# Performance work log

Hardware: AMD Instinct MI355X
Metric: run time of the kernel (lower is better)

Reference implementation:

```python
import jax, jax.numpy as jnp
import numpy as np

N = 50000      # num nodes
E = 40000      # num edges (multiple of BATCH)
BATCH = 200    # hardcoded edge batch size in source
ND, ED, TD, MD, D = 256, 128, 128, 256, 256
P = 4096       # num post nodes
EPS = 1e-16


def setup_inputs() -> dict:
    key = jax.random.key(0)
    ks = jax.random.split(key, 24)
    s = 0.02
    inp = {}
    inp["node_features"] = jax.random.normal(ks[0], (N, ND), jnp.float32)
    inp["edge_index"] = jax.random.randint(ks[1], (2, E), 0, N, jnp.int32)
    inp["edge_attr"] = jax.random.normal(ks[2], (E, ED), jnp.float32)
    inp["edge_times"] = jax.random.uniform(ks[3], (E,), jnp.float32)
    inp["post_mask"] = jax.random.randint(ks[4], (P,), 0, N, jnp.int32)
    # TimeEncoder('sin') params
    inp["w_time"] = jnp.ones((TD,), jnp.float32)
    inp["b_time"] = jnp.zeros((TD,), jnp.float32)
    # message_fn: Linear(ND+MD+ED+TD -> D), ReLU, Linear(D -> MD), ReLU
    min_dim = ND + MD + ED + TD
    inp["Wm1"] = s * jax.random.normal(ks[5], (min_dim, D), jnp.float32)
    inp["bm1"] = jnp.zeros((D,), jnp.float32)
    inp["Wm2"] = s * jax.random.normal(ks[6], (D, MD), jnp.float32)
    inp["bm2"] = jnp.zeros((MD,), jnp.float32)
    # GRUCell(MD, MD)
    inp["Wi"] = s * jax.random.normal(ks[7], (MD, 3 * MD), jnp.float32)
    inp["Wh"] = s * jax.random.normal(ks[8], (MD, 3 * MD), jnp.float32)
    inp["bi"] = jnp.zeros((3 * MD,), jnp.float32)
    inp["bh"] = jnp.zeros((3 * MD,), jnp.float32)
    # graph attention embedding: in = ND+MD+TD (augmented), edge feat = ED+TD
    inp["Wg"] = s * jax.random.normal(ks[9], (ND + MD + TD, D), jnp.float32)
    inp["We"] = s * jax.random.normal(ks[10], (ED + TD, D), jnp.float32)
    inp["a_src"] = s * jax.random.normal(ks[11], (D,), jnp.float32)
    inp["a_dst"] = s * jax.random.normal(ks[12], (D,), jnp.float32)
    inp["a_e"] = s * jax.random.normal(ks[13], (D,), jnp.float32)
    # classifier MLP: Linear(D -> D//2), ReLU, Linear(D//2 -> 1)
    inp["Wc1"] = s * jax.random.normal(ks[14], (D, D // 2), jnp.float32)
    inp["bc1"] = jnp.zeros((D // 2,), jnp.float32)
    inp["Wc2"] = s * jax.random.normal(ks[15], (D // 2, 1), jnp.float32)
    inp["bc2"] = jnp.zeros((1,), jnp.float32)
    return inp


def reference(node_features, edge_index, edge_attr, edge_times, post_mask,
              w_time, b_time, Wm1, bm1, Wm2, bm2, Wi, Wh, bi, bh,
              Wg, We, a_src, a_dst, a_e, Wc1, bc1, Wc2, bc2):
    def time_enc(t):  # TimeEncoder 'sin': sin(w * t + b)
        return jnp.sin(t[..., None] * w_time + b_time)

    # ---- time-sorted edge stream, batched in chunks of BATCH ----
    order = jnp.argsort(edge_times)
    nb = E // BATCH
    src_s = edge_index[0, order].reshape(nb, BATCH)
    ea_s = edge_attr[order].reshape(nb, BATCH, ED)
    t_s = edge_times[order].reshape(nb, BATCH)

    def step(mem, batch):
        src, ea, t = batch
        te = time_enc(t)                                   # [B, TD]
        h_prev = mem[src]                                  # [B, MD]
        x = jnp.concatenate([node_features[src], h_prev, ea, te], axis=-1)
        msg = jax.nn.relu(jax.nn.relu(x @ Wm1 + bm1) @ Wm2 + bm2)  # [B, MD]
        gi = msg @ Wi + bi
        gh = h_prev @ Wh + bh
        ir, iz, inn = jnp.split(gi, 3, axis=-1)
        hr, hz, hn = jnp.split(gh, 3, axis=-1)
        r = jax.nn.sigmoid(ir + hr)
        z = jax.nn.sigmoid(iz + hz)
        n = jnp.tanh(inn + r * hn)
        h_new = (1.0 - z) * n + z * h_prev
        mem = mem.at[src].set(h_new)
        return mem, None

    mem0 = jnp.zeros((N, MD), jnp.float32)
    mem, _ = jax.lax.scan(step, mem0, (src_s, ea_s, t_s))

    # ---- augmented node features with global time encoding ----
    gte = time_enc(jnp.max(edge_times))                    # [TD]
    gte = jnp.broadcast_to(gte, (N, TD))
    aug = jnp.concatenate([node_features, mem, gte], axis=1)  # [N, ND+MD+TD]

    # ---- graph attention embedding (single layer) ----
    h = aug @ Wg                                           # [N, D]
    ef = jnp.concatenate([edge_attr, time_enc(edge_times)], axis=1) @ We  # [E, D]
    s_idx, d_idx = edge_index[0], edge_index[1]
    logit = jax.nn.leaky_relu(
        (h @ a_src)[s_idx] + (h @ a_dst)[d_idx] + ef @ a_e, 0.2)  # [E]
    mx = jax.ops.segment_max(logit, d_idx, num_segments=N)
    mx = jnp.where(jnp.isfinite(mx), mx, 0.0)
    alpha = jnp.exp(logit - mx[d_idx])
    denom = jax.ops.segment_sum(alpha, d_idx, num_segments=N)     # [N]
    msg = alpha[:, None] * (h[s_idx] + ef)                        # [E, D]
    out = jax.ops.segment_sum(msg, d_idx, num_segments=N) / (denom[:, None] + EPS)

    # ---- classifier head on post nodes ----
    pe = out[post_mask]                                    # [P, D]
    logits = (jax.nn.relu(pe @ Wc1 + bc1) @ Wc2 + bc2)[:, 0]
    return jax.nn.sigmoid(logits)
```

## Files before the change

kernel.cpp:

```cpp
#include <hip/hip_runtime.h>

#define NN 50000
#define EE 40000
#define PP 4096
#define MAXR 12
#define SCAP 16
#define NB 65536
#define TANCH 2
#define TSTEPS 10
#define TGRID 512

typedef unsigned short us;
typedef __attribute__((ext_vector_type(8))) short bf8v;
typedef __attribute__((ext_vector_type(4))) float f4v;

__device__ __forceinline__ us f2b(float x) {
    unsigned u = __float_as_uint(x);
    u = (u + 0x7fffu + ((u >> 16) & 1u)) >> 16;
    return (us)u;
}
__device__ __forceinline__ float b2f(us h) {
    return __uint_as_float(((unsigned)h) << 16);
}
__device__ __forceinline__ unsigned fkey(float f) {
    unsigned u = __float_as_uint(f);
    return (u & 0x80000000u) ? ~u : (u | 0x80000000u);
}
__device__ __forceinline__ float funkey(unsigned k) {
    unsigned u = (k & 0x80000000u) ? (k & 0x7fffffffu) : ~k;
    return __uint_as_float(u);
}
__device__ __forceinline__ int bucket_of(float tv) {
    int b = (int)(tv * 65536.0f);
    if (b < 0) b = 0;
    if (b > 65535) b = 65535;
    return b;
}
__device__ __forceinline__ unsigned relu2bf(unsigned u) {
    unsigned lo = (u & 0x8000u) ? 0u : (u & 0xFFFFu);
    unsigned hi = (u & 0x80000000u) ? 0u : (u & 0xFFFF0000u);
    return lo | hi;
}


__global__ void k_need(const int* __restrict__ pm, int* __restrict__ needed)
{
    int i = blockIdx.x * 256 + threadIdx.x;
    if (i < PP) needed[pm[i]] = 1;
}

__global__ void k_elist(const int* __restrict__ src, const int* __restrict__ dst,
                        const int* __restrict__ needed, int* __restrict__ necnt,
                        int* __restrict__ eidx, int* __restrict__ uneed)
{
    __shared__ int lc, lb;
    if (threadIdx.x == 0) lc = 0;
    __syncthreads();
    int e = blockIdx.x * 256 + threadIdx.x;
    int slot = -1;
    if (e < EE && needed[dst[e]]) {
        slot = atomicAdd(&lc, 1);
        uneed[dst[e]] = 1;
        uneed[src[e]] = 1;
    }
    __syncthreads();
    if (threadIdx.x == 0 && lc) lb = atomicAdd(necnt, lc);
    __syncthreads();
    if (slot >= 0) eidx[lb + slot] = e;
}

__global__ void k_ulist(const int* __restrict__ uneed, int* __restrict__ ucnt,
                        int* __restrict__ ulist, int* __restrict__ nidx)
{
    __shared__ int lc, lb;
    if (threadIdx.x == 0) lc = 0;
    __syncthreads();
    int n = blockIdx.x * 256 + threadIdx.x;
    int slot = -1;
    if (n < NN && uneed[n]) slot = atomicAdd(&lc, 1);
    __syncthreads();
    if (threadIdx.x == 0 && lc) lb = atomicAdd(ucnt, lc);
    __syncthreads();
    if (slot >= 0) { ulist[lb + slot] = n; nidx[n] = lb + slot; }
}


__global__ __launch_bounds__(256) void k_prep(const float* __restrict__ t, const int* __restrict__ src,
                                              int* __restrict__ hist, int* __restrict__ scnt,
                                              int* __restrict__ slist, unsigned* __restrict__ tm)
{
    int e = blockIdx.x * 256 + threadIdx.x;
    float v = 0.f;
    if (e < EE) {
        float tv = t[e];
        v = tv;
        atomicAdd(&hist[bucket_of(tv)], 1);
        int s = src[e];
        int slot = atomicAdd(&scnt[s], 1);
        if (slot < SCAP) slist[s * SCAP + slot] = e;
    }
#pragma unroll
    for (int o = 32; o > 0; o >>= 1) v = fmaxf(v, __shfl_xor(v, o));
    if ((threadIdx.x & 63) == 0) atomicMax(tm, fkey(v));
}

__global__ void k_scan1(const int* __restrict__ hist, int* __restrict__ hbase, int* __restrict__ bsum)
{
    __shared__ int s[256];
    int i = blockIdx.x * 256 + threadIdx.x;
    int v = hist[i];
    s[threadIdx.x] = v;
    __syncthreads();
    for (int o = 1; o < 256; o <<= 1) {
        int x = (threadIdx.x >= o) ? s[threadIdx.x - o] : 0;
        __syncthreads();
        s[threadIdx.x] += x;
        __syncthreads();
    }
    hbase[i] = s[threadIdx.x] - v;
    if (threadIdx.x == 255) bsum[blockIdx.x] = s[255];
}

__global__ void k_scan2(int* __restrict__ bsum)
{
    __shared__ int s[256];
    int v = bsum[threadIdx.x];
    s[threadIdx.x] = v;
    __syncthreads();
    for (int o = 1; o < 256; o <<= 1) {
        int x = (threadIdx.x >= o) ? s[threadIdx.x - o] : 0;
        __syncthreads();
        s[threadIdx.x] += x;
        __syncthreads();
    }
    bsum[threadIdx.x] = s[threadIdx.x] - v;
}

__global__ void k_scan3(int* __restrict__ hbase, const int* __restrict__ bsum)
{
    int i = blockIdx.x * 256 + threadIdx.x;
    hbase[i] += bsum[blockIdx.x];
}

__global__ void k_bscatter(const float* __restrict__ t, const int* __restrict__ hbase,
                           int* __restrict__ hcur, int* __restrict__ blist)
{
    int e = blockIdx.x * 256 + threadIdx.x;
    if (e >= EE) return;
    int b = bucket_of(t[e]);
    int p = hbase[b] + atomicAdd(&hcur[b], 1);
    blist[p] = e;
}

__global__ void k_rank2(const float* __restrict__ t, const int* __restrict__ hbase,
                        const int* __restrict__ hist, const int* __restrict__ blist,
                        int* __restrict__ rank)
{
    int e = blockIdx.x * 256 + threadIdx.x;
    if (e >= EE) return;
    float te_ = t[e];
    int b = bucket_of(te_);
    int base = hbase[b], cnt = hist[b];
    int r = base;
    for (int i = 0; i < cnt; ++i) {
        int j = blist[base + i];
        float tj = t[j];
        r += (tj < te_ || (tj == te_ && j < e)) ? 1 : 0;
    }
    rank[e] = r;
}

__global__ void k_chain(const int* __restrict__ src, const int* __restrict__ rank,
                        const int* __restrict__ scnt, const int* __restrict__ slist,
                        const int* __restrict__ uneed,
                        int* __restrict__ roundcnt, int* __restrict__ roundx, int* __restrict__ roundsrc,
                        int* __restrict__ xcnt, int* __restrict__ xlist, int* __restrict__ xsrc)
{
    __shared__ int lcnt[MAXR];
    __shared__ int lbase[MAXR];
    __shared__ int xl, xb;
    int tid = threadIdx.x;
    if (tid < MAXR) lcnt[tid] = 0;
    if (tid == 0) xl = 0;
    __syncthreads();
    int e = blockIdx.x * 256 + tid;
    int pos = -1, slot = 0, xs = 0, ssave = 0;
    if (e < EE && uneed[src[e]]) {
        int s = src[e];
        int c = scnt[s]; if (c > SCAP) c = SCAP;
        int re = rank[e], be = re / 200;
        bool r_e = true;
        for (int i = 0; i < c; ++i) {
            int rj = rank[slist[s * SCAP + i]];
            if (rj / 200 == be && rj > re) { r_e = false; break; }
        }
        if (r_e) {
            int p = 0;
            for (int i = 0; i < c; ++i) {
                int rj = rank[slist[s * SCAP + i]];
                if (rj >= re) continue;
                int bj = rj / 200;
                bool r_j = true;
                for (int k2 = 0; k2 < c; ++k2) {
                    int rj2 = rank[slist[s * SCAP + k2]];
                    if (rj2 / 200 == bj && rj2 > rj) { r_j = false; break; }
                }
                p += r_j ? 1 : 0;
            }
            if (p < MAXR) { pos = p; ssave = s; slot = atomicAdd(&lcnt[p], 1); xs = atomicAdd(&xl, 1); }
        }
    }
    __syncthreads();
    if (tid < MAXR && lcnt[tid]) lbase[tid] = atomicAdd(&roundcnt[tid], lcnt[tid]);
    if (tid == 0 && xl) xb = atomicAdd(xcnt, xl);
    __syncthreads();
    if (pos >= 0) {
        int xr = xb + xs;
        xlist[xr] = e;
        xsrc[xr] = ssave;
        size_t o = (size_t)pos * EE + lbase[pos] + slot;
        roundx[o] = xr;
        roundsrc[o] = ssave;
    }
}


__global__ void k_zmem(const int* __restrict__ ucnt, const int* __restrict__ ulist,
                       float* __restrict__ memb, us* __restrict__ memb_bf)
{
    int total = *ucnt * 64;
    for (int i = blockIdx.x * 256 + threadIdx.x; i < total; i += gridDim.x * 256) {
        int n = ulist[i >> 6], q = i & 63;
        reinterpret_cast<float4*>(memb + (size_t)n * 256)[q] = make_float4(0.f, 0.f, 0.f, 0.f);
        reinterpret_cast<ushort4*>(memb_bf + (size_t)n * 256)[q] = make_ushort4(0, 0, 0, 0);
    }
}

__global__ void k_cvtg(const int* __restrict__ ucnt, const int* __restrict__ ulist,
                       const float* __restrict__ nf, us* __restrict__ nf_bf)
{
    int total = *ucnt * 64;
    for (int i = blockIdx.x * 256 + threadIdx.x; i < total; i += gridDim.x * 256) {
        int n = ulist[i >> 6], q = i & 63;
        float4 v = reinterpret_cast<const float4*>(nf + (size_t)n * 256)[q];
        ushort4 o; o.x = f2b(v.x); o.y = f2b(v.y); o.z = f2b(v.z); o.w = f2b(v.w);
        reinterpret_cast<ushort4*>(nf_bf + (size_t)n * 256)[q] = o;
    }
}

__global__ void k_convL(const int* __restrict__ cnt, const int* __restrict__ list,
                        const float* __restrict__ t, const float* __restrict__ w,
                        const float* __restrict__ b, us* __restrict__ te,
                        const float* __restrict__ ea, us* __restrict__ ea_bf)
{
    int total = *cnt * 32;
    for (int i = blockIdx.x * 256 + threadIdx.x; i < total; i += gridDim.x * 256) {
        int e = list[i >> 5], q = (i & 31) * 4;
        float tv = t[e];
        ushort4 ot;
        ot.x = f2b(sinf(tv * w[q] + b[q]));
        ot.y = f2b(sinf(tv * w[q + 1] + b[q + 1]));
        ot.z = f2b(sinf(tv * w[q + 2] + b[q + 2]));
        ot.w = f2b(sinf(tv * w[q + 3] + b[q + 3]));
        *reinterpret_cast<ushort4*>(te + (size_t)e * 128 + q) = ot;
        float4 v = *reinterpret_cast<const float4*>(ea + (size_t)e * 128 + q);
        ushort4 oa; oa.x = f2b(v.x); oa.y = f2b(v.y); oa.z = f2b(v.z); oa.w = f2b(v.w);
        *reinterpret_cast<ushort4*>(ea_bf + (size_t)e * 128 + q) = oa;
    }
}

__global__ void k_zout(const int* __restrict__ pm, float* __restrict__ outb,
                       float* __restrict__ denom, unsigned* __restrict__ mx)
{
    int i = blockIdx.x * 256 + threadIdx.x;
    int p = i >> 6, q = i & 63;
    if (p >= PP) return;
    int n = pm[p];
    reinterpret_cast<float4*>(outb + (size_t)n * 256)[q] = make_float4(0.f, 0.f, 0.f, 0.f);
    if (q == 0) { denom[n] = 0.f; mx[n] = 0u; }
}

__global__ void k_wkflat(const float* __restrict__ sa, us* __restrict__ da, int na4,
                         const float* __restrict__ sb, us* __restrict__ db, int nb4,
                         const float* __restrict__ sc, us* __restrict__ dc, int nc4,
                         const float* __restrict__ sd, us* __restrict__ dd, int nd4)
{
    int i = blockIdx.x * 256 + threadIdx.x;
    const float* sp; us* dp; int j = i;
    if (j < na4) { sp = sa; dp = da; }
    else { j -= na4; if (j < nb4) { sp = sb; dp = db; }
    else { j -= nb4; if (j < nc4) { sp = sc; dp = dc; }
    else { j -= nc4; if (j < nd4) { sp = sd; dp = dd; } else return; } } }
    float4 v = reinterpret_cast<const float4*>(sp)[j];
    ushort4 o; o.x = f2b(v.x); o.y = f2b(v.y); o.z = f2b(v.z); o.w = f2b(v.w);
    reinterpret_cast<ushort4*>(dp)[j] = o;
}


struct WtD { const float* W; us* dst; int K, N, ld, koff, Ktot, toff; };
struct WtA { WtD d[12]; int ntiles; };

__global__ __launch_bounds__(256) void k_wt2(WtA wa, const unsigned* __restrict__ tm,
                                             const float* __restrict__ wt, const float* __restrict__ bt,
                                             const float* __restrict__ Wg, float* __restrict__ gvec)
{
    if ((int)blockIdx.x == wa.ntiles) {
        __shared__ float sv[128];
        int c = threadIdx.x;
        float tmax = funkey(*tm);
        if (c < 128) sv[c] = sinf(tmax * wt[c] + bt[c]);
        __syncthreads();
        float acc = 0.f;
        for (int k = 0; k < 128; ++k) acc += sv[k] * Wg[(size_t)(512 + k) * 256 + c];
        gvec[c] = acc;
        return;
    }
    int bid = blockIdx.x;
    int di = 0;
#pragma unroll
    for (int i = 1; i < 12; ++i) if (bid >= wa.d[i].toff) di = i;
    WtD d = wa.d[di];
    int tt = bid - d.toff;
    int tn = d.N >> 5;
    int k0 = (tt / tn) << 5, n0 = (tt % tn) << 5;
    __shared__ float ld[32][33];
    int tx = threadIdx.x & 31, ty = threadIdx.x >> 5;
#pragma unroll
    for (int i = 0; i < 4; ++i)
        ld[ty + 8 * i][tx] = d.W[(size_t)(k0 + ty + 8 * i) * d.ld + n0 + tx];
    __syncthreads();
#pragma unroll
    for (int i = 0; i < 4; ++i) {
        int n = n0 + ty + 8 * i;
        d.dst[(size_t)n * d.Ktot + d.koff + k0 + tx] = f2b(ld[tx][ty + 8 * i]);
    }
}

__global__ __launch_bounds__(256) void k_mgemm(
    const us* __restrict__ A1, int K1, const int* __restrict__ idx1,
    const us* __restrict__ A2, int K2, const int* __restrict__ idx2,
    const us* __restrict__ A3, int K3, const int* __restrict__ idx3,
    const us* __restrict__ Wt, int Kloop, int ldw,
    const float* __restrict__ bias,
    const us* __restrict__ Cin, const int* __restrict__ cidx,
    float* __restrict__ outF, us* __restrict__ outB, int ldc,
    int Mhost, const int* __restrict__ mdev, int mbase, int relu, int relua)
{
    int M = Mhost;
    if (mdev) {
        int avail = *mdev - mbase;
        if (avail < 0) avail = 0;
        if (avail < M) M = avail;
    }
    const int row0 = blockIdx.x * 128;
    if (row0 >= M) return;
    const int col0 = blockIdx.y * 64;

    __shared__ us As[128 * 64];
    __shared__ us Bs[64 * 64];

    const int tid = threadIdx.x;
    const int l = tid & 63;
    const int wv = tid >> 6;

    f4v acc[2][4];
#pragma unroll
    for (int i = 0; i < 2; ++i)
#pragma unroll
        for (int j = 0; j < 4; ++j) acc[i][j] = (f4v){0.f, 0.f, 0.f, 0.f};

    for (int k0 = 0; k0 < Kloop; k0 += 64) {
#pragma unroll
        for (int it = 0; it < 4; ++it) {
            int idx = tid + it * 256;
            int r = idx >> 3, q = idx & 7;
            int gk = k0 + q * 8;
            int grow = row0 + r;
            uint4 v = make_uint4(0u, 0u, 0u, 0u);
            if (grow < M) {
                const us* sp; int st, krel, ar = grow;
                if (gk < K1) {
                    sp = A1; st = K1; krel = gk;
                    if (idx1) ar = idx1[ar];
                } else if (gk < K1 + K2) {
                    sp = A2; st = K2; krel = gk - K1;
                    if (idx2) ar = idx2[ar];
                } else {
                    sp = A3; st = K3; krel = gk - K1 - K2;
                    if (idx3) ar = idx3[ar];
                }
                v = *reinterpret_cast<const uint4*>(sp + (size_t)ar * st + krel);
                if (relua) { v.x = relu2bf(v.x); v.y = relu2bf(v.y); v.z = relu2bf(v.z); v.w = relu2bf(v.w); }
            }
            *reinterpret_cast<uint4*>(As + r * 64 + ((q ^ (r & 7)) << 3)) = v;
        }
#pragma unroll
        for (int it = 0; it < 2; ++it) {
            int idx = tid + it * 256;
            int c = idx >> 3, q = idx & 7;
            uint4 v = *reinterpret_cast<const uint4*>(Wt + (size_t)(col0 + c) * ldw + k0 + q * 8);
            *reinterpret_cast<uint4*>(Bs + c * 64 + ((q ^ (c & 7)) << 3)) = v;
        }
        __syncthreads();
#pragma unroll
        for (int ks = 0; ks < 2; ++ks) {
            bf8v af[2], bfr[4];
#pragma unroll
            for (int mf = 0; mf < 2; ++mf) {
                int r = wv * 32 + mf * 16 + (l & 15);
                int q = ks * 4 + (l >> 4);
                af[mf] = *reinterpret_cast<const bf8v*>(As + r * 64 + ((q ^ (r & 7)) << 3));
            }
#pragma unroll
            for (int nf = 0; nf < 4; ++nf) {
                int c = nf * 16 + (l & 15);
                int q = ks * 4 + (l >> 4);
                bfr[nf] = *reinterpret_cast<const bf8v*>(Bs + c * 64 + ((q ^ (c & 7)) << 3));
            }
#pragma unroll
            for (int mf = 0; mf < 2; ++mf)
#pragma unroll
                for (int nf = 0; nf < 4; ++nf)
                    acc[mf][nf] = __builtin_amdgcn_mfma_f32_16x16x32_bf16(af[mf], bfr[nf], acc[mf][nf], 0, 0, 0);
        }
        __syncthreads();
    }

#pragma unroll
    for (int mf = 0; mf < 2; ++mf) {
#pragma unroll
        for (int rr = 0; rr < 4; ++rr) {
            int row = row0 + wv * 32 + mf * 16 + ((l >> 4) * 4) + rr;
            if (row >= M) continue;
            size_t crow = 0;
            if (Cin) crow = (size_t)(cidx ? cidx[row] : row) * ldc;
#pragma unroll
            for (int nf = 0; nf < 4; ++nf) {
                int col = col0 + nf * 16 + (l & 15);
                float v = acc[mf][nf][rr];
                if (bias) v += bias[col];
                if (Cin) v += b2f(Cin[crow + col]);
                if (relu) v = fmaxf(v, 0.f);
                if (outF) outF[(size_t)row * ldc + col] = v;
                if (outB) outB[(size_t)row * ldc + col] = f2b(v);
            }
        }
    }
}


__global__ void k_hgather(const int* __restrict__ cnt, int cb, int m, const int* __restrict__ rs,
                          const us* __restrict__ mem_bf, us* __restrict__ hprev)
{
    int idx = blockIdx.x * 256 + threadIdx.x;
    int i = idx >> 6, q = idx & 63;
    int avail = *cnt - cb;
    if (avail > m) avail = m;
    if (i >= avail) return;
    int s = rs[i];
    reinterpret_cast<ushort4*>(hprev + (size_t)i * 256)[q] =
        reinterpret_cast<const ushort4*>(mem_bf + (size_t)s * 256)[q];
}

__global__ void k_gate(const int* __restrict__ cnt, int cb, int m, const int* __restrict__ rs,
                       const us* __restrict__ gates, const float* __restrict__ bi,
                       const float* __restrict__ bh,
                       float* __restrict__ mem, us* __restrict__ mem_bf)
{
    int avail = *cnt - cb;
    if (avail > m) avail = m;
    int c = threadIdx.x;
    for (int i = blockIdx.x; i < avail; i += gridDim.x) {
        int s = rs[i];
        float hp = mem[(size_t)s * 256 + c];
        const us* g = gates + (size_t)i * 1024;
        float g0 = b2f(g[c]) + bi[c] + bh[c];
        float g1 = b2f(g[256 + c]) + bi[256 + c] + bh[256 + c];
        float g2i = b2f(g[512 + c]) + bi[512 + c];
        float g2h = b2f(g[768 + c]) + bh[512 + c];
        float r = 1.f / (1.f + expf(-g0));
        float z = 1.f / (1.f + expf(-g1));
        float n = tanhf(g2i + r * g2h);
        float hnew = (1.f - z) * n + z * hp;
        mem[(size_t)s * 256 + c] = hnew;
        mem_bf[(size_t)s * 256 + c] = f2b(hnew);
    }
}

__global__ void k_tbuild(const int* __restrict__ roundcnt, const int* __restrict__ roundx,
                         const int* __restrict__ roundsrc, int* __restrict__ tx)
{
    int i = blockIdx.x * 256 + threadIdx.x;
    if (i >= roundcnt[TANCH]) return;
    int s = roundsrc[(size_t)TANCH * EE + i];
    tx[i * TSTEPS + 0] = roundx[(size_t)TANCH * EE + i];
#pragma unroll
    for (int k = 1; k < TSTEPS; ++k) tx[i * TSTEPS + k] = -1;
    for (int j = TANCH + 1; j < MAXR; ++j) {
        int cj = roundcnt[j];
        for (int m2 = 0; m2 < cj; ++m2) {
            if (roundsrc[(size_t)j * EE + m2] == s) {
                tx[i * TSTEPS + (j - TANCH)] = roundx[(size_t)j * EE + m2];
                break;
            }
        }
    }
}

__global__ __launch_bounds__(1024) void k_tailchain(
    const int* __restrict__ roundcnt, const int* __restrict__ roundsrc, const int* __restrict__ tx,
    const us* __restrict__ xpart_c, const us* __restrict__ Wk_a, const us* __restrict__ Wk_m2,
    const us* __restrict__ Wk_i, const us* __restrict__ Wk_h, const float* __restrict__ bm2,
    const float* __restrict__ bi, const float* __restrict__ bh,
    float* __restrict__ mem, us* __restrict__ mem_bf)
{
    const int cnt = roundcnt[TANCH];
    const int tid = threadIdx.x;
    const int c = tid & 255;
    const int p = tid >> 8;
    __shared__ float hb[256];
    __shared__ float xv[256];
    __shared__ float msgv[256];
    __shared__ float red[4][256];
    __shared__ float oi[768];
    __shared__ float oh[768];
    for (int i = blockIdx.x; i < cnt; i += gridDim.x) {
        int s = roundsrc[(size_t)TANCH * EE + i];
        float hp = 0.f;
        if (p == 0) { hp = mem[(size_t)s * 256 + c]; hb[c] = hp; }
        __syncthreads();
        for (int k = 0; k < TSTEPS; ++k) {
            int xr = tx[i * TSTEPS + k];
            if (xr < 0) break;
            {
                float a = 0.f;
                int k0 = p * 64;
#pragma unroll 16
                for (int kk = 0; kk < 64; ++kk) a += b2f(Wk_a[(size_t)(k0 + kk) * 256 + c]) * hb[k0 + kk];
                red[p][c] = a;
            }
            __syncthreads();
            if (p == 0)
                xv[c] = fmaxf(b2f(xpart_c[(size_t)xr * 256 + c]) + red[0][c] + red[1][c] + red[2][c] + red[3][c], 0.f);
            __syncthreads();
            {
                float a = 0.f;
                int k0 = p * 64;
#pragma unroll 16
                for (int kk = 0; kk < 64; ++kk) a += b2f(Wk_m2[(size_t)(k0 + kk) * 256 + c]) * xv[k0 + kk];
                red[p][c] = a;
            }
            __syncthreads();
            if (p == 0)
                msgv[c] = fmaxf(bm2[c] + red[0][c] + red[1][c] + red[2][c] + red[3][c], 0.f);
            __syncthreads();
            if (tid < 768) {
                float a = 0.f;
#pragma unroll 16
                for (int kk = 0; kk < 256; ++kk) a += b2f(Wk_i[(size_t)kk * 768 + tid]) * msgv[kk];
                oi[tid] = a;
            } else {
                int j = tid - 768;
                float a = 0.f;
#pragma unroll 16
                for (int kk = 0; kk < 256; ++kk) a += b2f(Wk_h[(size_t)kk * 768 + j]) * hb[kk];
                oh[j] = a;
            }
            if (tid < 512) {
                int j = 256 + tid;
                float a = 0.f;
#pragma unroll 16
                for (int kk = 0; kk < 256; ++kk) a += b2f(Wk_h[(size_t)kk * 768 + j]) * hb[kk];
                oh[j] = a;
            }
            __syncthreads();
            if (p == 0) {
                float r = 1.f / (1.f + expf(-(oi[c] + oh[c] + bi[c] + bh[c])));
                float z = 1.f / (1.f + expf(-(oi[256 + c] + oh[256 + c] + bi[256 + c] + bh[256 + c])));
                float n = tanhf((oi[512 + c] + bi[512 + c]) + r * (oh[512 + c] + bh[512 + c]));
                hp = (1.f - z) * n + z * hp;
                hb[c] = hp;
            }
            __syncthreads();
        }
        if (p == 0) {
            mem[(size_t)s * 256 + c] = hp;
            mem_bf[(size_t)s * 256 + c] = f2b(hp);
        }
        __syncthreads();
    }
}


__global__ __launch_bounds__(256) void k_dots(const us* __restrict__ hc, const us* __restrict__ efc,
                                              const int* __restrict__ ucnt, const int* __restrict__ necnt,
                                              const float* __restrict__ v_s, const float* __restrict__ v_d,
                                              const float* __restrict__ v_e,
                                              float* __restrict__ sdot, float* __restrict__ ddot,
                                              float* __restrict__ edot)
{
    int lane = threadIdx.x & 63;
    int row = blockIdx.x * 4 + (threadIdx.x >> 6);
    if (row < NN) {
        if (row >= *ucnt) return;
        ushort4 q = reinterpret_cast<const ushort4*>(hc + (size_t)row * 256)[lane];
        int c = lane * 4;
        float x0 = b2f(q.x), x1 = b2f(q.y), x2 = b2f(q.z), x3 = b2f(q.w);
        float s1 = x0 * v_s[c] + x1 * v_s[c + 1] + x2 * v_s[c + 2] + x3 * v_s[c + 3];
        float s2 = x0 * v_d[c] + x1 * v_d[c + 1] + x2 * v_d[c + 2] + x3 * v_d[c + 3];
#pragma unroll
        for (int o = 32; o > 0; o >>= 1) { s1 += __shfl_xor(s1, o); s2 += __shfl_xor(s2, o); }
        if (lane == 0) { sdot[row] = s1; ddot[row] = s2; }
    } else {
        int i = row - NN;
        if (i >= *necnt) return;
        ushort4 q = reinterpret_cast<const ushort4*>(efc + (size_t)i * 256)[lane];
        int c = lane * 4;
        float s1 = b2f(q.x) * v_e[c] + b2f(q.y) * v_e[c + 1] + b2f(q.z) * v_e[c + 2] + b2f(q.w) * v_e[c + 3];
#pragma unroll
        for (int o = 32; o > 0; o >>= 1) s1 += __shfl_xor(s1, o);
        if (lane == 0) edot[i] = s1;
    }
}

__global__ void k_logitc(const int* __restrict__ necnt, const int* __restrict__ eidx,
                         const int* __restrict__ nidx,
                         const float* __restrict__ sdot, const float* __restrict__ ddot,
                         const float* __restrict__ edot, const int* __restrict__ src,
                         const int* __restrict__ dst, float* __restrict__ logit,
                         unsigned* __restrict__ mx)
{
    int i = blockIdx.x * 256 + threadIdx.x;
    if (i >= *necnt) return;
    int e = eidx[i];
    float l = sdot[nidx[src[e]]] + ddot[nidx[dst[e]]] + edot[i];
    l = (l > 0.f) ? l : 0.2f * l;
    logit[i] = l;
    atomicMax(&mx[dst[e]], fkey(l));
}

__global__ void k_alphac(const int* __restrict__ necnt, const int* __restrict__ eidx,
                         const float* __restrict__ logit, const int* __restrict__ dst,
                         const unsigned* __restrict__ mx, float* __restrict__ alpha,
                         float* __restrict__ denom)
{
    int i = blockIdx.x * 256 + threadIdx.x;
    if (i >= *necnt) return;
    int d = dst[eidx[i]];
    float a = expf(logit[i] - funkey(mx[d]));
    alpha[i] = a;
    atomicAdd(&denom[d], a);
}

__global__ void k_scatc(const int* __restrict__ necnt, const int* __restrict__ eidx,
                        const int* __restrict__ nidx,
                        const float* __restrict__ alpha, const int* __restrict__ src,
                        const int* __restrict__ dst, const us* __restrict__ hc,
                        const us* __restrict__ efc, float* __restrict__ outb)
{
    int i = blockIdx.x * 4 + (threadIdx.x >> 6);
    if (i >= *necnt) return;
    int c4 = threadIdx.x & 63;
    int e = eidx[i];
    float a = alpha[i];
    ushort4 hv = reinterpret_cast<const ushort4*>(hc + (size_t)nidx[src[e]] * 256)[c4];
    ushort4 ev = reinterpret_cast<const ushort4*>(efc + (size_t)i * 256)[c4];
    float* op = outb + (size_t)dst[e] * 256 + c4 * 4;
    atomicAdd(op + 0, a * (b2f(hv.x) + b2f(ev.x)));
    atomicAdd(op + 1, a * (b2f(hv.y) + b2f(ev.y)));
    atomicAdd(op + 2, a * (b2f(hv.z) + b2f(ev.z)));
    atomicAdd(op + 3, a * (b2f(hv.w) + b2f(ev.w)));
}

__global__ void k_pe(const int* __restrict__ pm, const float* __restrict__ outb,
                     const float* __restrict__ denom, us* __restrict__ pe)
{
    int p = blockIdx.x, c = threadIdx.x;
    int n = pm[p];
    pe[(size_t)p * 256 + c] = f2b(outb[(size_t)n * 256 + c] / (denom[n] + 1e-16f));
}

__global__ __launch_bounds__(256) void k_final(const float* __restrict__ c1, const float* __restrict__ Wc2,
                                               const float* __restrict__ bc2, float* __restrict__ out)
{
    int lane = threadIdx.x & 63;
    int row = blockIdx.x * 4 + (threadIdx.x >> 6);
    if (row >= PP) return;
    float s = 0.f;
    for (int c = lane; c < 128; c += 64) s += c1[(size_t)row * 128 + c] * Wc2[c];
#pragma unroll
    for (int off = 32; off > 0; off >>= 1) s += __shfl_xor(s, off);
    if (lane == 0) out[row] = 1.f / (1.f + expf(-(s + bc2[0])));
}


extern "C" void kernel_launch(void* const* d_in, const int* in_sizes, int n_in,
                              void* d_out, int out_size, void* d_ws, size_t ws_size,
                              hipStream_t stream)
{
    (void)in_sizes; (void)n_in; (void)out_size;
    const float* nf    = (const float*)d_in[0];
    const int*   ei    = (const int*)  d_in[1];
    const float* ea    = (const float*)d_in[2];
    const float* t     = (const float*)d_in[3];
    const int*   pm    = (const int*)  d_in[4];
    const float* wt    = (const float*)d_in[5];
    const float* bt    = (const float*)d_in[6];
    const float* Wm1   = (const float*)d_in[7];
    const float* bm1   = (const float*)d_in[8];
    const float* Wm2   = (const float*)d_in[9];
    const float* bm2   = (const float*)d_in[10];
    const float* Wi    = (const float*)d_in[11];
    const float* Wh    = (const float*)d_in[12];
    const float* bi    = (const float*)d_in[13];
    const float* bh    = (const float*)d_in[14];
    const float* Wg    = (const float*)d_in[15];
    const float* We    = (const float*)d_in[16];
    const float* a_src = (const float*)d_in[17];
    const float* a_dst = (const float*)d_in[18];
    const float* a_e   = (const float*)d_in[19];
    const float* Wc1   = (const float*)d_in[20];
    const float* bc1   = (const float*)d_in[21];
    const float* Wc2   = (const float*)d_in[22];
    const float* bc2   = (const float*)d_in[23];
    float* outp = (float*)d_out;
    const int* src = ei;
    const int* dst = ei + EE;

    char* base = (char*)d_ws;
    size_t off = 0;
    auto alloc = [&](size_t bytes) -> void* {
        void* p = base + off;
        off = (off + bytes + 255) & ~(size_t)255;
        return p;
    };
    int* rank      = (int*)alloc((size_t)EE * 4);
    int* roundcnt  = (int*)alloc(64 * 4);
    int* roundx    = (int*)alloc((size_t)MAXR * EE * 4);
    int* roundsrc  = (int*)alloc((size_t)MAXR * EE * 4);
    int* bsum      = (int*)alloc(256 * 4);
    int* eidx      = (int*)alloc((size_t)EE * 4);
    int* xlist     = (int*)alloc((size_t)EE * 4);
    int* xsrc      = (int*)alloc((size_t)EE * 4);
    int* tx        = (int*)alloc((size_t)TSTEPS * (EE / 3 + 256) * 4);
    int* ulist     = (int*)alloc((size_t)NN * 4);
    int* nidx      = (int*)alloc((size_t)NN * 4);
    us* te_bf    = (us*)alloc((size_t)EE * 128 * 2);
    us* nf_bf    = (us*)alloc((size_t)NN * 256 * 2);
    us* ea_bf    = (us*)alloc((size_t)EE * 128 * 2);
    us* xh       = (us*)alloc((size_t)NN * 256 * 2);
    float* memb  = (float*)alloc((size_t)NN * 256 * 4);
    us* memb_bf  = (us*)alloc((size_t)NN * 256 * 2);
    us* Wt_x    = (us*)alloc((size_t)256 * 512 * 2);
    us* Wt_a    = (us*)alloc((size_t)256 * 256 * 2);
    us* Wt_m2   = (us*)alloc((size_t)256 * 256 * 2);
    us* Wt_gate = (us*)alloc((size_t)1024 * 512 * 2);
    us* Wt_g    = (us*)alloc((size_t)256 * 512 * 2);
    us* Wt_e    = (us*)alloc((size_t)256 * 256 * 2);
    us* Wt_c    = (us*)alloc((size_t)128 * 256 * 2);
    us* Wk_a    = (us*)alloc((size_t)256 * 256 * 2);
    us* Wk_m2   = (us*)alloc((size_t)256 * 256 * 2);
    us* Wk_i    = (us*)alloc((size_t)256 * 768 * 2);
    us* Wk_h    = (us*)alloc((size_t)256 * 768 * 2);
    float* gvec  = (float*)alloc(256 * 4);
    float* sdot  = (float*)alloc((size_t)NN * 4);
    float* ddot  = (float*)alloc((size_t)NN * 4);
    float* edot  = (float*)alloc((size_t)EE * 4);
    float* logit = (float*)alloc((size_t)EE * 4);
    float* alpha = (float*)alloc((size_t)EE * 4);
    unsigned* mx = (unsigned*)alloc((size_t)NN * 4);
    float* denom = (float*)alloc((size_t)NN * 4);
    int* needed  = (int*)alloc((size_t)NN * 4);
    int* uneed   = (int*)alloc((size_t)NN * 4);
    int* scnt    = (int*)alloc((size_t)NN * 4);
    char* zone_end = base + off;

    size_t region = (ws_size > off + 4096) ? (ws_size - off - 4096) : 0;
    long capL = (long)(region / 3584);
    int CAPR = (int)(capL < 0 ? 0 : capL);
    CAPR = (CAPR / 128) * 128;
    if (CAPR > 28160) CAPR = 28160;
    if (CAPR < 1280) return;
    us* xbuf_bf  = (us*)alloc((size_t)CAPR * 256 * 2);
    us* msg_bf   = (us*)alloc((size_t)CAPR * 256 * 2);
    us* hprev_c  = (us*)alloc((size_t)CAPR * 256 * 2);
    us* gates_bf = (us*)alloc((size_t)CAPR * 1024 * 2);
    if (off > ws_size) return;

    unsigned* tm = (unsigned*)&roundcnt[32];
    int* necnt   = &roundcnt[33];
    int* ucnt    = &roundcnt[34];
    int* xcnt    = &roundcnt[35];
    int* hist  = roundx;
    int* hcur  = roundx + NB;
    int* hbase = roundx + 2 * NB;
    int* blist = roundx + 3 * NB;
    int* slist = (int*)xh;
    us* xpart_c = xh;
    us* hc = xh;
    us* ef_c = nf_bf;
    float* outb = memb;
    us* pe_bf = te_bf;
    float* c1 = (float*)(te_bf + (size_t)PP * 256);

    const dim3 B(256);
    const int gE = (EE + 255) / 256;
    const int gN = (NN + 255) / 256;

    hipMemsetAsync(roundcnt, 0, 64 * 4, stream);
    hipMemsetAsync(hist, 0, (size_t)2 * NB * 4, stream);
    hipMemsetAsync(needed, 0, (size_t)(zone_end - (char*)needed), stream);
    hipMemsetAsync(Wt_gate, 0, (size_t)1024 * 512 * 2, stream);

    k_need<<<(PP + 255) / 256, B, 0, stream>>>(pm, needed);
    k_elist<<<gE, B, 0, stream>>>(src, dst, needed, necnt, eidx, uneed);
    k_ulist<<<gN, B, 0, stream>>>(uneed, ucnt, ulist, nidx);

    k_prep<<<gE, B, 0, stream>>>(t, src, hist, scnt, slist, tm);
    k_scan1<<<256, B, 0, stream>>>(hist, hbase, bsum);
    k_scan2<<<1, B, 0, stream>>>(bsum);
    k_scan3<<<256, B, 0, stream>>>(hbase, bsum);
    k_bscatter<<<gE, B, 0, stream>>>(t, hbase, hcur, blist);
    k_rank2<<<gE, B, 0, stream>>>(t, hbase, hist, blist, rank);
    k_chain<<<gE, B, 0, stream>>>(src, rank, scnt, slist, uneed, roundcnt, roundx, roundsrc,
                                  xcnt, xlist, xsrc);

    k_zmem<<<1024, B, 0, stream>>>(ucnt, ulist, memb, memb_bf);
    k_cvtg<<<1024, B, 0, stream>>>(ucnt, ulist, nf, nf_bf);
    k_convL<<<1024, B, 0, stream>>>(xcnt, xlist, t, wt, bt, te_bf, ea, ea_bf);
    k_convL<<<1024, B, 0, stream>>>(necnt, eidx, t, wt, bt, te_bf, ea, ea_bf);

    {
        int na4 = 256 * 256 / 4, nb4 = 256 * 256 / 4, nc4 = 256 * 768 / 4, nd4 = 256 * 768 / 4;
        int tot = na4 + nb4 + nc4 + nd4;
        k_wkflat<<<(tot + 255) / 256, B, 0, stream>>>(
            Wm1 + (size_t)256 * 256, Wk_a, na4, Wm2, Wk_m2, nb4, Wi, Wk_i, nc4, Wh, Wk_h, nd4);
    }

    {
        WtA wa;
        int o = 0;
        auto set = [&](int i, const float* W, us* dstp, int K, int N, int ld, int koff, int Ktot) {
            wa.d[i] = WtD{W, dstp, K, N, ld, koff, Ktot, o};
            o += (K >> 5) * (N >> 5);
        };
        set(0, Wm1, Wt_x, 256, 256, 256, 0, 512);
        set(1, Wm1 + (size_t)512 * 256, Wt_x, 128, 256, 256, 256, 512);
        set(2, Wm1 + (size_t)640 * 256, Wt_x, 128, 256, 256, 384, 512);
        set(3, Wm1 + (size_t)256 * 256, Wt_a, 256, 256, 256, 0, 256);
        set(4, Wm2, Wt_m2, 256, 256, 256, 0, 256);
        set(5, Wi, Wt_gate, 256, 512, 768, 0, 512);
        set(6, Wh, Wt_gate, 256, 512, 768, 256, 512);
        set(7, Wi + 512, Wt_gate + (size_t)512 * 512, 256, 256, 768, 0, 512);
        set(8, Wh + 512, Wt_gate + (size_t)768 * 512, 256, 256, 768, 256, 512);
        set(9, Wg, Wt_g, 512, 256, 256, 0, 512);
        set(10, We, Wt_e, 256, 256, 256, 0, 256);
        set(11, Wc1, Wt_c, 256, 128, 128, 0, 256);
        wa.ntiles = o;
        k_wt2<<<o + 1, B, 0, stream>>>(wa, tm, wt, bt, Wg, gvec);
    }

    const int gxE = (EE + 127) / 128;
    k_mgemm<<<dim3(gxE, 4), B, 0, stream>>>(nf_bf, 256, xsrc, ea_bf, 128, xlist,
        te_bf, 128, xlist, Wt_x, 512, 512, bm1, nullptr, nullptr,
        nullptr, xpart_c, 256, EE, xcnt, 0, 0, 0);

    for (int j = 0; j < TANCH; ++j) {
        int bound = EE / 4;
        for (int cb = 0; cb < bound; cb += CAPR) {
            int m = bound - cb; if (m > CAPR) m = CAPR;
            int gx = (m + 127) / 128;
            const int* rx = roundx + (size_t)j * EE + cb;
            const int* rs = roundsrc + (size_t)j * EE + cb;
            if (j == 0) {
                k_mgemm<<<dim3(gx, 4), B, 0, stream>>>(xpart_c, 256, rx, nullptr, 0, nullptr,
                    nullptr, 0, nullptr, Wt_m2, 256, 256, bm2, nullptr, nullptr,
                    nullptr, msg_bf, 256, m, roundcnt + j, cb, 1, 1);
                k_mgemm<<<dim3(gx, 16), B, 0, stream>>>(msg_bf, 256, nullptr, nullptr, 0, nullptr,
                    nullptr, 0, nullptr, Wt_gate, 256, 512, nullptr, nullptr, nullptr,
                    nullptr, gates_bf, 1024, m, roundcnt + j, cb, 0, 0);
            } else {
                k_hgather<<<(m * 64 + 255) / 256, B, 0, stream>>>(roundcnt + j, cb, m, rs, memb_bf, hprev_c);
                k_mgemm<<<dim3(gx, 4), B, 0, stream>>>(hprev_c, 256, nullptr, nullptr, 0, nullptr,
                    nullptr, 0, nullptr, Wt_a, 256, 256, nullptr, xpart_c, rx,
                    nullptr, xbuf_bf, 256, m, roundcnt + j, cb, 1, 0);
                k_mgemm<<<dim3(gx, 4), B, 0, stream>>>(xbuf_bf, 256, nullptr, nullptr, 0, nullptr,
                    nullptr, 0, nullptr, Wt_m2, 256, 256, bm2, nullptr, nullptr,
                    nullptr, msg_bf, 256, m, roundcnt + j, cb, 1, 0);
                k_mgemm<<<dim3(gx, 16), B, 0, stream>>>(msg_bf, 256, nullptr, hprev_c, 256, nullptr,
                    nullptr, 0, nullptr, Wt_gate, 512, 512, nullptr, nullptr, nullptr,
                    nullptr, gates_bf, 1024, m, roundcnt + j, cb, 0, 0);
            }
            k_gate<<<2048, B, 0, stream>>>(roundcnt + j, cb, m, rs, gates_bf, bi, bh, memb, memb_bf);
        }
    }
    k_tbuild<<<(EE / 3 + 255) / 256, B, 0, stream>>>(roundcnt, roundx, roundsrc, tx);
    k_tailchain<<<TGRID, dim3(1024), 0, stream>>>(roundcnt, roundsrc, tx, xpart_c,
                                                  Wk_a, Wk_m2, Wk_i, Wk_h,
                                                  bm2, bi, bh, memb, memb_bf);

    k_zout<<<(PP * 64 + 255) / 256, B, 0, stream>>>(pm, outb, denom, mx);

    const int gxN = (NN + 127) / 128;
    k_mgemm<<<dim3(gxN, 4), B, 0, stream>>>(nf_bf, 256, ulist, memb_bf, 256, ulist,
        nullptr, 0, nullptr, Wt_g, 512, 512, gvec, nullptr, nullptr,
        nullptr, hc, 256, NN, ucnt, 0, 0, 0);

    k_mgemm<<<dim3(gxE, 4), B, 0, stream>>>(ea_bf, 128, eidx, te_bf, 128, eidx,
        nullptr, 0, nullptr, Wt_e, 256, 256, nullptr, nullptr, nullptr,
        nullptr, ef_c, 256, EE, necnt, 0, 0, 0);

    k_dots<<<(NN + EE + 3) / 4, B, 0, stream>>>(hc, ef_c, ucnt, necnt, a_src, a_dst, a_e, sdot, ddot, edot);

    k_logitc<<<gE, B, 0, stream>>>(necnt, eidx, nidx, sdot, ddot, edot, src, dst, logit, mx);
    k_alphac<<<gE, B, 0, stream>>>(necnt, eidx, logit, dst, mx, alpha, denom);
    k_scatc<<<(EE + 3) / 4, B, 0, stream>>>(necnt, eidx, nidx, alpha, src, dst, hc, ef_c, outb);

    k_pe<<<PP, B, 0, stream>>>(pm, outb, denom, pe_bf);
    k_mgemm<<<dim3((PP + 127) / 128, 2), B, 0, stream>>>(pe_bf, 256, nullptr, nullptr, 0, nullptr,
        nullptr, 0, nullptr, Wt_c, 256, 256, bc1, nullptr, nullptr,
        c1, nullptr, 128, PP, nullptr, 0, 1, 0);
    k_final<<<(PP + 3) / 4, B, 0, stream>>>(c1, Wc2, bc2, outp);
}
```

Before: 470.5 us.

## Merge small setup kernels, shrink time histogram, interleave GRU weights in tail chain

Folds the post-mask marking into the prep kernel and cuts the time histogram from 65536 to 8192 buckets, so a single-block scan replaces the three-kernel scan. It also merges the zero-memory and node-convert kernels and the two edge-convert launches, reducing launch count. The tail-chain kernel now reads bf16 weight pairs as 32-bit words and uses eight k-partitions, and it interleaves the Wi and Wh weights so one loop computes both GRU projections. Coarser buckets put more edges in each bucket, which may make the rank step inside a bucket more expensive.

```diff
diff --git a/kernel.cpp b/kernel.cpp
--- a/kernel.cpp
+++ b/kernel.cpp
@@ -5,7 +5,7 @@
 #define PP 4096
 #define MAXR 12
 #define SCAP 16
-#define NB 65536
+#define NB 8192
 #define TANCH 2
 #define TSTEPS 10
 #define TGRID 512
@@ -31,9 +31,9 @@
     return __uint_as_float(u);
 }
 __device__ __forceinline__ int bucket_of(float tv) {
-    int b = (int)(tv * 65536.0f);
+    int b = (int)(tv * 8192.0f);
     if (b < 0) b = 0;
-    if (b > 65535) b = 65535;
+    if (b > NB - 1) b = NB - 1;
     return b;
 }
 __device__ __forceinline__ unsigned relu2bf(unsigned u) {
@@ -42,12 +42,6 @@
     return lo | hi;
 }
 
-
-__global__ void k_need(const int* __restrict__ pm, int* __restrict__ needed)
-{
-    int i = blockIdx.x * 256 + threadIdx.x;
-    if (i < PP) needed[pm[i]] = 1;
-}
 
 __global__ void k_elist(const int* __restrict__ src, const int* __restrict__ dst,
                         const int* __restrict__ needed, int* __restrict__ necnt,
@@ -85,11 +79,17 @@
 }
 
 
-__global__ __launch_bounds__(256) void k_prep(const float* __restrict__ t, const int* __restrict__ src,
+__global__ __launch_bounds__(256) void k_prep(const int* __restrict__ pm, int* __restrict__ needed,
+                                              const float* __restrict__ t, const int* __restrict__ src,
                                               int* __restrict__ hist, int* __restrict__ scnt,
                                               int* __restrict__ slist, unsigned* __restrict__ tm)
 {
-    int e = blockIdx.x * 256 + threadIdx.x;
+    if (blockIdx.x < 16) {
+        int i = blockIdx.x * 256 + threadIdx.x;
+        if (i < PP) needed[pm[i]] = 1;
+        return;
+    }
+    int e = (blockIdx.x - 16) * 256 + threadIdx.x;
     float v = 0.f;
     if (e < EE) {
         float tv = t[e];
@@ -104,42 +104,26 @@
     if ((threadIdx.x & 63) == 0) atomicMax(tm, fkey(v));
 }
 
-__global__ void k_scan1(const int* __restrict__ hist, int* __restrict__ hbase, int* __restrict__ bsum)
-{
-    __shared__ int s[256];
-    int i = blockIdx.x * 256 + threadIdx.x;
-    int v = hist[i];
-    s[threadIdx.x] = v;
+__global__ __launch_bounds__(256) void k_scanone(const int* __restrict__ hist, int* __restrict__ hbase)
+{
+    __shared__ int tot[256];
+    int t = threadIdx.x;
+    int base = t * (NB / 256);
+    int loc[NB / 256];
+    int s = 0;
+#pragma unroll
+    for (int i = 0; i < NB / 256; ++i) { loc[i] = s; s += hist[base + i]; }
+    tot[t] = s;
     __syncthreads();
     for (int o = 1; o < 256; o <<= 1) {
-        int x = (threadIdx.x >= o) ? s[threadIdx.x - o] : 0;
+        int x = (t >= o) ? tot[t - o] : 0;
         __syncthreads();
-        s[threadIdx.x] += x;
+        tot[t] += x;
         __syncthreads();
     }
-    hbase[i] = s[threadIdx.x] - v;
-    if (threadIdx.x == 255) bsum[blockIdx.x] = s[255];
-}
-
-__global__ void k_scan2(int* __restrict__ bsum)
-{
-    __shared__ int s[256];
-    int v = bsum[threadIdx.x];
-    s[threadIdx.x] = v;
-    __syncthreads();
-    for (int o = 1; o < 256; o <<= 1) {
-        int x = (threadIdx.x >= o) ? s[threadIdx.x - o] : 0;
-        __syncthreads();
-        s[threadIdx.x] += x;
-        __syncthreads();
-    }
-    bsum[threadIdx.x] = s[threadIdx.x] - v;
-}
-
-__global__ void k_scan3(int* __restrict__ hbase, const int* __restrict__ bsum)
-{
-    int i = blockIdx.x * 256 + threadIdx.x;
-    hbase[i] += bsum[blockIdx.x];
+    int off = tot[t] - s;
+#pragma unroll
+    for (int i = 0; i < NB / 256; ++i) hbase[base + i] = loc[i] + off;
 }
 
 __global__ void k_bscatter(const float* __restrict__ t, const int* __restrict__ hbase,
@@ -225,7 +209,8 @@
 }
 
 
-__global__ void k_zmem(const int* __restrict__ ucnt, const int* __restrict__ ulist,
+__global__ void k_zcvt(const int* __restrict__ ucnt, const int* __restrict__ ulist,
+                       const float* __restrict__ nf, us* __restrict__ nf_bf,
                        float* __restrict__ memb, us* __restrict__ memb_bf)
 {
     int total = *ucnt * 64;
@@ -233,29 +218,25 @@
         int n = ulist[i >> 6], q = i & 63;
         reinterpret_cast<float4*>(memb + (size_t)n * 256)[q] = make_float4(0.f, 0.f, 0.f, 0.f);
         reinterpret_cast<ushort4*>(memb_bf + (size_t)n * 256)[q] = make_ushort4(0, 0, 0, 0);
-    }
-}
-
-__global__ void k_cvtg(const int* __restrict__ ucnt, const int* __restrict__ ulist,
-                       const float* __restrict__ nf, us* __restrict__ nf_bf)
-{
-    int total = *ucnt * 64;
-    for (int i = blockIdx.x * 256 + threadIdx.x; i < total; i += gridDim.x * 256) {
-        int n = ulist[i >> 6], q = i & 63;
         float4 v = reinterpret_cast<const float4*>(nf + (size_t)n * 256)[q];
         ushort4 o; o.x = f2b(v.x); o.y = f2b(v.y); o.z = f2b(v.z); o.w = f2b(v.w);
         reinterpret_cast<ushort4*>(nf_bf + (size_t)n * 256)[q] = o;
     }
 }
 
-__global__ void k_convL(const int* __restrict__ cnt, const int* __restrict__ list,
-                        const float* __restrict__ t, const float* __restrict__ w,
-                        const float* __restrict__ b, us* __restrict__ te,
-                        const float* __restrict__ ea, us* __restrict__ ea_bf)
-{
-    int total = *cnt * 32;
+__global__ void k_convL2(const int* __restrict__ xcnt, const int* __restrict__ xlist,
+                         const int* __restrict__ necnt, const int* __restrict__ eidx,
+                         const float* __restrict__ t, const float* __restrict__ w,
+                         const float* __restrict__ b, us* __restrict__ te,
+                         const float* __restrict__ ea, us* __restrict__ ea_bf)
+{
+    int t1 = *xcnt * 32, t2 = *necnt * 32;
+    int total = t1 + t2;
     for (int i = blockIdx.x * 256 + threadIdx.x; i < total; i += gridDim.x * 256) {
-        int e = list[i >> 5], q = (i & 31) * 4;
+        int ii = i;
+        const int* lst = xlist;
+        if (ii >= t1) { ii -= t1; lst = eidx; }
+        int e = lst[ii >> 5], q = (ii & 31) * 4;
         float tv = t[e];
         ushort4 ot;
         ot.x = f2b(sinf(tv * w[q] + b[q]));
@@ -282,18 +263,30 @@
 
 __global__ void k_wkflat(const float* __restrict__ sa, us* __restrict__ da, int na4,
                          const float* __restrict__ sb, us* __restrict__ db, int nb4,
-                         const float* __restrict__ sc, us* __restrict__ dc, int nc4,
-                         const float* __restrict__ sd, us* __restrict__ dd, int nd4)
+                         const float* __restrict__ Wi, const float* __restrict__ Wh,
+                         us* __restrict__ Wk_ih, int nih)
 {
     int i = blockIdx.x * 256 + threadIdx.x;
-    const float* sp; us* dp; int j = i;
-    if (j < na4) { sp = sa; dp = da; }
-    else { j -= na4; if (j < nb4) { sp = sb; dp = db; }
-    else { j -= nb4; if (j < nc4) { sp = sc; dp = dc; }
-    else { j -= nc4; if (j < nd4) { sp = sd; dp = dd; } else return; } } }
-    float4 v = reinterpret_cast<const float4*>(sp)[j];
-    ushort4 o; o.x = f2b(v.x); o.y = f2b(v.y); o.z = f2b(v.z); o.w = f2b(v.w);
-    reinterpret_cast<ushort4*>(dp)[j] = o;
+    int j = i;
+    if (j < na4) {
+        float4 v = reinterpret_cast<const float4*>(sa)[j];
+        ushort4 o; o.x = f2b(v.x); o.y = f2b(v.y); o.z = f2b(v.z); o.w = f2b(v.w);
+        reinterpret_cast<ushort4*>(da)[j] = o;
+        return;
+    }
+    j -= na4;
+    if (j < nb4) {
+        float4 v = reinterpret_cast<const float4*>(sb)[j];
+        ushort4 o; o.x = f2b(v.x); o.y = f2b(v.y); o.z = f2b(v.z); o.w = f2b(v.w);
+        reinterpret_cast<ushort4*>(db)[j] = o;
+        return;
+    }
+    j -= nb4;
+    if (j < nih) {
+        unsigned lo = (unsigned)f2b(Wi[j]);
+        unsigned hi = (unsigned)f2b(Wh[j]);
+        reinterpret_cast<unsigned*>(Wk_ih)[j] = lo | (hi << 16);
+    }
 }
 
 
@@ -510,7 +503,7 @@
 __global__ __launch_bounds__(1024) void k_tailchain(
     const int* __restrict__ roundcnt, const int* __restrict__ roundsrc, const int* __restrict__ tx,
     const us* __restrict__ xpart_c, const us* __restrict__ Wk_a, const us* __restrict__ Wk_m2,
-    const us* __restrict__ Wk_i, const us* __restrict__ Wk_h, const float* __restrict__ bm2,
+    const us* __restrict__ Wk_ih, const float* __restrict__ bm2,
     const float* __restrict__ bi, const float* __restrict__ bh,
     float* __restrict__ mem, us* __restrict__ mem_bf)
 {
@@ -518,10 +511,12 @@
     const int tid = threadIdx.x;
     const int c = tid & 255;
     const int p = tid >> 8;
+    const int c2 = (tid & 127) * 2;
+    const int kp = tid >> 7;
     __shared__ float hb[256];
     __shared__ float xv[256];
     __shared__ float msgv[256];
-    __shared__ float red[4][256];
+    __shared__ float red[8][256];
     __shared__ float oi[768];
     __shared__ float oh[768];
     for (int i = blockIdx.x; i < cnt; i += gridDim.x) {
@@ -533,45 +528,57 @@
             int xr = tx[i * TSTEPS + k];
             if (xr < 0) break;
             {
-                float a = 0.f;
-                int k0 = p * 64;
+                float a0 = 0.f, a1 = 0.f;
+                int k0 = kp * 32;
 #pragma unroll 16
-                for (int kk = 0; kk < 64; ++kk) a += b2f(Wk_a[(size_t)(k0 + kk) * 256 + c]) * hb[k0 + kk];
-                red[p][c] = a;
+                for (int kk = 0; kk < 32; ++kk) {
+                    unsigned w = *reinterpret_cast<const unsigned*>(Wk_a + (size_t)(k0 + kk) * 256 + c2);
+                    float hv = hb[k0 + kk];
+                    a0 += b2f((us)(w & 0xffffu)) * hv;
+                    a1 += b2f((us)(w >> 16)) * hv;
+                }
+                red[kp][c2] = a0;
+                red[kp][c2 + 1] = a1;
             }
             __syncthreads();
-            if (p == 0)
-                xv[c] = fmaxf(b2f(xpart_c[(size_t)xr * 256 + c]) + red[0][c] + red[1][c] + red[2][c] + red[3][c], 0.f);
+            if (p == 0) {
+                float a = b2f(xpart_c[(size_t)xr * 256 + c]);
+#pragma unroll
+                for (int r8 = 0; r8 < 8; ++r8) a += red[r8][c];
+                xv[c] = fmaxf(a, 0.f);
+            }
             __syncthreads();
             {
-                float a = 0.f;
-                int k0 = p * 64;
+                float a0 = 0.f, a1 = 0.f;
+                int k0 = kp * 32;
 #pragma unroll 16
-                for (int kk = 0; kk < 64; ++kk) a += b2f(Wk_m2[(size_t)(k0 + kk) * 256 + c]) * xv[k0 + kk];
-                red[p][c] = a;
+                for (int kk = 0; kk < 32; ++kk) {
+                    unsigned w = *reinterpret_cast<const unsigned*>(Wk_m2 + (size_t)(k0 + kk) * 256 + c2);
+                    float hv = xv[k0 + kk];
+                    a0 += b2f((us)(w & 0xffffu)) * hv;
+                    a1 += b2f((us)(w >> 16)) * hv;
+                }
+                red[kp][c2] = a0;
+                red[kp][c2 + 1] = a1;
             }
             __syncthreads();
-            if (p == 0)
-                msgv[c] = fmaxf(bm2[c] + red[0][c] + red[1][c] + red[2][c] + red[3][c], 0.f);
+            if (p == 0) {
+                float a = bm2[c];
+#pragma unroll
+                for (int r8 = 0; r8 < 8; ++r8) a += red[r8][c];
+                msgv[c] = fmaxf(a, 0.f);
+            }
             __syncthreads();
             if (tid < 768) {
-                float a = 0.f;
+                float ai = 0.f, ah = 0.f;
 #pragma unroll 16
-                for (int kk = 0; kk < 256; ++kk) a += b2f(Wk_i[(size_t)kk * 768 + tid]) * msgv[kk];
-                oi[tid] = a;
-            } else {
-                int j = tid - 768;
-                float a = 0.f;
-#pragma unroll 16
-                for (int kk = 0; kk < 256; ++kk) a += b2f(Wk_h[(size_t)kk * 768 + j]) * hb[kk];
-                oh[j] = a;
-            }
-            if (tid < 512) {
-                int j = 256 + tid;
-                float a = 0.f;
-#pragma unroll 16
-                for (int kk = 0; kk < 256; ++kk) a += b2f(Wk_h[(size_t)kk * 768 + j]) * hb[kk];
-                oh[j] = a;
+                for (int kk = 0; kk < 256; ++kk) {
+                    unsigned w = reinterpret_cast<const unsigned*>(Wk_ih)[(size_t)kk * 768 + tid];
+                    ai += b2f((us)(w & 0xffffu)) * msgv[kk];
+                    ah += b2f((us)(w >> 16)) * hb[kk];
+                }
+                oi[tid] = ai;
+                oh[tid] = ah;
             }
             __syncthreads();
             if (p == 0) {
@@ -738,7 +745,6 @@
     int* roundcnt  = (int*)alloc(64 * 4);
     int* roundx    = (int*)alloc((size_t)MAXR * EE * 4);
     int* roundsrc  = (int*)alloc((size_t)MAXR * EE * 4);
-    int* bsum      = (int*)alloc(256 * 4);
     int* eidx      = (int*)alloc((size_t)EE * 4);
     int* xlist     = (int*)alloc((size_t)EE * 4);
     int* xsrc      = (int*)alloc((size_t)EE * 4);
@@ -760,8 +766,7 @@
     us* Wt_c    = (us*)alloc((size_t)128 * 256 * 2);
     us* Wk_a    = (us*)alloc((size_t)256 * 256 * 2);
     us* Wk_m2   = (us*)alloc((size_t)256 * 256 * 2);
-    us* Wk_i    = (us*)alloc((size_t)256 * 768 * 2);
-    us* Wk_h    = (us*)alloc((size_t)256 * 768 * 2);
+    us* Wk_ih   = (us*)alloc((size_t)256 * 768 * 2 * 2);
     float* gvec  = (float*)alloc(256 * 4);
     float* sdot  = (float*)alloc((size_t)NN * 4);
     float* ddot  = (float*)alloc((size_t)NN * 4);
@@ -812,29 +817,24 @@
     hipMemsetAsync(needed, 0, (size_t)(zone_end - (char*)needed), stream);
     hipMemsetAsync(Wt_gate, 0, (size_t)1024 * 512 * 2, stream);
 
-    k_need<<<(PP + 255) / 256, B, 0, stream>>>(pm, needed);
+    k_prep<<<16 + gE, B, 0, stream>>>(pm, needed, t, src, hist, scnt, slist, tm);
     k_elist<<<gE, B, 0, stream>>>(src, dst, needed, necnt, eidx, uneed);
     k_ulist<<<gN, B, 0, stream>>>(uneed, ucnt, ulist, nidx);
 
-    k_prep<<<gE, B, 0, stream>>>(t, src, hist, scnt, slist, tm);
-    k_scan1<<<256, B, 0, stream>>>(hist, hbase, bsum);
-    k_scan2<<<1, B, 0, stream>>>(bsum);
-    k_scan3<<<256, B, 0, stream>>>(hbase, bsum);
+    k_scanone<<<1, B, 0, stream>>>(hist, hbase);
     k_bscatter<<<gE, B, 0, stream>>>(t, hbase, hcur, blist);
     k_rank2<<<gE, B, 0, stream>>>(t, hbase, hist, blist, rank);
     k_chain<<<gE, B, 0, stream>>>(src, rank, scnt, slist, uneed, roundcnt, roundx, roundsrc,
                                   xcnt, xlist, xsrc);
 
-    k_zmem<<<1024, B, 0, stream>>>(ucnt, ulist, memb, memb_bf);
-    k_cvtg<<<1024, B, 0, stream>>>(ucnt, ulist, nf, nf_bf);
-    k_convL<<<1024, B, 0, stream>>>(xcnt, xlist, t, wt, bt, te_bf, ea, ea_bf);
-    k_convL<<<1024, B, 0, stream>>>(necnt, eidx, t, wt, bt, te_bf, ea, ea_bf);
+    k_zcvt<<<1024, B, 0, stream>>>(ucnt, ulist, nf, nf_bf, memb, memb_bf);
+    k_convL2<<<1024, B, 0, stream>>>(xcnt, xlist, necnt, eidx, t, wt, bt, te_bf, ea, ea_bf);
 
     {
-        int na4 = 256 * 256 / 4, nb4 = 256 * 256 / 4, nc4 = 256 * 768 / 4, nd4 = 256 * 768 / 4;
-        int tot = na4 + nb4 + nc4 + nd4;
+        int na4 = 256 * 256 / 4, nb4 = 256 * 256 / 4, nih = 256 * 768;
+        int tot = na4 + nb4 + nih;
         k_wkflat<<<(tot + 255) / 256, B, 0, stream>>>(
-            Wm1 + (size_t)256 * 256, Wk_a, na4, Wm2, Wk_m2, nb4, Wi, Wk_i, nc4, Wh, Wk_h, nd4);
+            Wm1 + (size_t)256 * 256, Wk_a, na4, Wm2, Wk_m2, nb4, Wi, Wh, Wk_ih, nih);
     }
 
     {
@@ -896,7 +896,7 @@
     }
     k_tbuild<<<(EE / 3 + 255) / 256, B, 0, stream>>>(roundcnt, roundx, roundsrc, tx);
     k_tailchain<<<TGRID, dim3(1024), 0, stream>>>(roundcnt, roundsrc, tx, xpart_c,
-                                                  Wk_a, Wk_m2, Wk_i, Wk_h,
+                                                  Wk_a, Wk_m2, Wk_ih,
                                                   bm2, bi, bh, memb, memb_bf);
 
     k_zout<<<(PP * 64 + 255) / 256, B, 0, stream>>>(pm, outb, denom, mx);
```

New measurement: 432.9 us. -8.0%, faster.
